# Optimization experiments

Hardware: AMD Instinct MI355X
Metric: run time of the kernel (lower is better)

Reference implementation:

```python
import jax, jax.numpy as jnp
import numpy as np

N, E = 20000, 320000
IN, HID, H, C, DFF, L = 256, 64, 4, 64, 128, 4  # per-head dim C = out_channels, concat width = H*C


def _init(k, shape, fan):
    return jax.random.normal(k, shape, jnp.float32) / np.float32(np.sqrt(fan))


def setup_inputs() -> dict:
    key = jax.random.key(0)
    ks = jax.random.split(key, 10)
    x = jax.random.normal(ks[0], (N, IN), jnp.float32)
    edge_index = jax.random.randint(ks[1], (2, E), 0, N)
    We = _init(ks[2], (IN, HID), IN)
    be = jnp.zeros((HID,), jnp.float32)
    Wc = _init(ks[3], (L, HID, H * C), HID)
    att_src = _init(ks[4], (L, H, C), C)
    att_dst = _init(ks[5], (L, H, C), C)
    bc = jnp.zeros((L, H * C), jnp.float32)
    W1 = _init(ks[6], (L, H * C, DFF), H * C)
    b1 = jnp.zeros((L, DFF), jnp.float32)
    W2 = _init(ks[7], (L, DFF, HID), DFF)
    b2 = jnp.zeros((L, HID), jnp.float32)
    ln_g = jnp.ones((L, HID), jnp.float32)
    ln_b = jnp.zeros((L, HID), jnp.float32)
    return dict(x=x, edge_index=edge_index, We=We, be=be, Wc=Wc, att_src=att_src,
                att_dst=att_dst, bc=bc, W1=W1, b1=b1, W2=W2, b2=b2, ln_g=ln_g, ln_b=ln_b)


def _layernorm(x, g, b, eps=1e-5):
    m = x.mean(-1, keepdims=True)
    v = ((x - m) ** 2).mean(-1, keepdims=True)
    return (x - m) / jnp.sqrt(v + eps) * g + b


def reference(x, edge_index, We, be, Wc, att_src, att_dst, bc, W1, b1, W2, b2, ln_g, ln_b):
    # dropout omitted (eval mode)
    n = x.shape[0]
    loops = jnp.arange(n, dtype=edge_index.dtype)
    src = jnp.concatenate([edge_index[0], loops])  # GATConv add_self_loops=True
    dst = jnp.concatenate([edge_index[1], loops])
    h = (x @ We + be) * jnp.sqrt(jnp.float32(HID))  # embed * sqrt(hidden)
    for l in range(L):  # small fixed layer loop
        xh = (h @ Wc[l]).reshape(n, H, C)          # [n,H,C]
        a_s = (xh * att_src[l]).sum(-1)            # [n,H]
        a_d = (xh * att_dst[l]).sum(-1)
        e = a_s[src] + a_d[dst]                    # [E+n,H]
        e = jnp.where(e > 0, e, 0.2 * e)           # leaky_relu(0.2)
        m = jax.ops.segment_max(e, dst, num_segments=n)
        e = jnp.exp(e - m[dst])
        z = jax.ops.segment_sum(e, dst, num_segments=n)
        alpha = e / (z[dst] + 1e-16)               # segment softmax over incoming edges
        msg = xh[src] * alpha[:, :, None]          # [E+n,H,C]
        out = jax.ops.segment_sum(msg, dst, num_segments=n).reshape(n, H * C) + bc[l]
        f = jax.nn.gelu(out @ W1[l] + b1[l], approximate=False) @ W2[l] + b2[l]
        h = h + _layernorm(f, ln_g[l], ln_b[l])    # residual
    return h  # last_hidden_state (head is None)
```

## Files before the change

### kernel.cpp

```cpp
#include <hip/hip_runtime.h>
#include <cmath>

#define NN   20000
#define NE   320000
#define IND  256
#define HIDD 64
#define NH   4
#define CD   64
#define HC   256
#define DFFD 128
#define NL   4


static __device__ __forceinline__ float lrelu(float v) { return v > 0.f ? v : 0.2f * v; }
static __device__ __forceinline__ float wsum(float v) { for (int k = 32; k; k >>= 1) v += __shfl_xor(v, k); return v; }
static __device__ __forceinline__ float wmax(float v) { for (int k = 32; k; k >>= 1) v = fmaxf(v, __shfl_xor(v, k)); return v; }

__global__ void ws_kernel(const float* __restrict__ Wc, const float* __restrict__ att_src,
                          const float* __restrict__ att_dst, float* __restrict__ ws_all) {
    int idx = blockIdx.x * 256 + threadIdx.x;
    int l = idx >> 9, r = (idx >> 6) & 7, k = idx & 63;
    int hh = r & 3;
    const float* att = ((r & 4) ? att_dst : att_src) + (size_t)l * NH * CD + hh * CD;
    const float* wrow = Wc + (size_t)l * HIDD * HC + (size_t)k * HC + hh * CD;
    float s = 0.f;
    for (int c = 0; c < CD; ++c) s += wrow[c] * att[c];
    ws_all[idx] = s;
}

__global__ __launch_bounds__(256) void embed_kernel(const float* __restrict__ x,
                                                    const float* __restrict__ We,
                                                    const float* __restrict__ be,
                                                    const float* __restrict__ ws_all,
                                                    float* __restrict__ h,
                                                    float* __restrict__ a_s, float* __restrict__ a_d) {
    __shared__ float s_x[16 * IND];
    const int base = blockIdx.x * 16, t = threadIdx.x;
    for (int idx = t; idx < 16 * IND / 4; idx += 256)
        ((float4*)s_x)[idx] = ((const float4*)(x + (size_t)base * IND))[idx];
    __syncthreads();
    const int c = t & 63, g = t >> 6;
    float acc[4] = {0.f, 0.f, 0.f, 0.f};
    const float4* sx4 = (const float4*)s_x;
#pragma unroll 2
    for (int k4 = 0; k4 < IND / 4; ++k4) {
        float w0 = We[(4 * k4 + 0) * HIDD + c];
        float w1 = We[(4 * k4 + 1) * HIDD + c];
        float w2 = We[(4 * k4 + 2) * HIDD + c];
        float w3 = We[(4 * k4 + 3) * HIDD + c];
#pragma unroll
        for (int i = 0; i < 4; ++i) {
            float4 v = sx4[(4 * g + i) * (IND / 4) + k4];
            acc[i] += v.x * w0 + v.y * w1 + v.z * w2 + v.w * w3;
        }
    }
    float bias = be[c];
    float wr[8];
#pragma unroll
    for (int r = 0; r < 8; ++r) wr[r] = ws_all[r * 64 + c];
#pragma unroll
    for (int i = 0; i < 4; ++i) {
        int node = base + 4 * g + i;
        float hv = (acc[i] + bias) * 8.0f;
        h[(size_t)node * HIDD + c] = hv;
        float s0 = wsum(hv * wr[0]), s1 = wsum(hv * wr[1]);
        float s2 = wsum(hv * wr[2]), s3 = wsum(hv * wr[3]);
        float s4 = wsum(hv * wr[4]), s5 = wsum(hv * wr[5]);
        float s6 = wsum(hv * wr[6]), s7 = wsum(hv * wr[7]);
        if (c == 0) {
            ((float4*)a_s)[node] = make_float4(s0, s1, s2, s3);
            ((float4*)a_d)[node] = make_float4(s4, s5, s6, s7);
        }
    }
}

__global__ void init_deg(int* __restrict__ deg, int* __restrict__ cursor) {
    int i = blockIdx.x * blockDim.x + threadIdx.x;
    if (i < NN) { deg[i] = 1; cursor[i] = 0; }
}

__global__ void count_edges(const int* __restrict__ ei, int* __restrict__ deg) {
    int e = blockIdx.x * blockDim.x + threadIdx.x;
    if (e < NE) atomicAdd(&deg[ei[NE + e]], 1);
}

__global__ void scan_kernel(const int* __restrict__ deg, int* __restrict__ rowptr) {
    __shared__ int part[1024];
    const int t = threadIdx.x;
    const int CH = (NN + 1023) / 1024;
    int lo = t * CH, hi = lo + CH; if (hi > NN) hi = NN;
    int s = 0;
    for (int i = lo; i < hi; ++i) s += deg[i];
    part[t] = s;
    __syncthreads();
    for (int off = 1; off < 1024; off <<= 1) {
        int v = 0;
        if (t >= off) v = part[t - off];
        __syncthreads();
        if (t >= off) part[t] += v;
        __syncthreads();
    }
    int base = (t == 0) ? 0 : part[t - 1];
    for (int i = lo; i < hi; ++i) { rowptr[i] = base; base += deg[i]; }
    if (lo <= NN - 1 && NN - 1 < hi) rowptr[NN] = base;
}

__global__ void scatter_edges(const int* __restrict__ ei, const int* __restrict__ rowptr,
                              int* __restrict__ cursor, int* __restrict__ csr_src) {
    int e = blockIdx.x * blockDim.x + threadIdx.x;
    if (e < NE) {
        int s = ei[e], d = ei[NE + e];
        int pos = atomicAdd(&cursor[d], 1);
        csr_src[rowptr[d] + pos] = s;
    } else if (e < NE + NN) {
        int i = e - NE;
        int pos = atomicAdd(&cursor[i], 1);
        csr_src[rowptr[i] + pos] = i;
    }
}

__global__ __launch_bounds__(256) void agg_kernel(
    const float* __restrict__ h, const float* __restrict__ a_s, const float* __restrict__ a_d,
    const int* __restrict__ rowptr, const int* __restrict__ csr_src,
    float* __restrict__ hagg) {
    __shared__ int    s_src[8][64];
    __shared__ float4 s_w[8][64];
    const int t = threadIdx.x, wave = t >> 6, lane = t & 63;
    const float4* as4 = (const float4*)a_s;
#pragma unroll
    for (int nd = 0; nd < 2; ++nd) {
        const int slot = wave * 2 + nd;
        const int i = blockIdx.x * 8 + slot;
        const int lo = rowptr[i], n = rowptr[i + 1] - lo;
        const float4 ad = ((const float4*)a_d)[i];
        float acc0 = 0.f, acc1 = 0.f, acc2 = 0.f, acc3 = 0.f;
        if (n <= 64) {
            float e0 = -1e30f, e1 = -1e30f, e2 = -1e30f, e3 = -1e30f;
            if (lane < n) {
                int s = csr_src[lo + lane];
                s_src[slot][lane] = s;
                float4 a = as4[s];
                e0 = lrelu(a.x + ad.x); e1 = lrelu(a.y + ad.y);
                e2 = lrelu(a.z + ad.z); e3 = lrelu(a.w + ad.w);
            }
            float M0 = wmax(e0), M1 = wmax(e1), M2 = wmax(e2), M3 = wmax(e3);
            float p0 = __expf(e0 - M0), p1 = __expf(e1 - M1);
            float p2 = __expf(e2 - M2), p3 = __expf(e3 - M3);
            float iz0 = 1.f / (wsum(p0) + 1e-16f), iz1 = 1.f / (wsum(p1) + 1e-16f);
            float iz2 = 1.f / (wsum(p2) + 1e-16f), iz3 = 1.f / (wsum(p3) + 1e-16f);
            if (lane < n) s_w[slot][lane] = make_float4(p0 * iz0, p1 * iz1, p2 * iz2, p3 * iz3);
            int j = 0;
            for (; j + 4 <= n; j += 4) {
                int  q0 = s_src[slot][j],     q1 = s_src[slot][j + 1];
                int  q2 = s_src[slot][j + 2], q3 = s_src[slot][j + 3];
                float h0 = h[(size_t)q0 * HIDD + lane], h1 = h[(size_t)q1 * HIDD + lane];
                float h2 = h[(size_t)q2 * HIDD + lane], h3 = h[(size_t)q3 * HIDD + lane];
                float4 w0 = s_w[slot][j],     w1 = s_w[slot][j + 1];
                float4 w2 = s_w[slot][j + 2], w3 = s_w[slot][j + 3];
                acc0 += h0 * w0.x + h1 * w1.x + h2 * w2.x + h3 * w3.x;
                acc1 += h0 * w0.y + h1 * w1.y + h2 * w2.y + h3 * w3.y;
                acc2 += h0 * w0.z + h1 * w1.z + h2 * w2.z + h3 * w3.z;
                acc3 += h0 * w0.w + h1 * w1.w + h2 * w2.w + h3 * w3.w;
            }
            for (; j < n; ++j) {
                float hv = h[(size_t)s_src[slot][j] * HIDD + lane];
                float4 w = s_w[slot][j];
                acc0 += hv * w.x; acc1 += hv * w.y; acc2 += hv * w.z; acc3 += hv * w.w;
            }
        } else {
            float m0 = -1e30f, m1 = -1e30f, m2 = -1e30f, m3 = -1e30f;
            for (int j = lane; j < n; j += 64) {
                int s = csr_src[lo + j];
                float4 a = as4[s];
                m0 = fmaxf(m0, lrelu(a.x + ad.x)); m1 = fmaxf(m1, lrelu(a.y + ad.y));
                m2 = fmaxf(m2, lrelu(a.z + ad.z)); m3 = fmaxf(m3, lrelu(a.w + ad.w));
            }
            m0 = wmax(m0); m1 = wmax(m1); m2 = wmax(m2); m3 = wmax(m3);
            float z0 = 0.f, z1 = 0.f, z2 = 0.f, z3 = 0.f;
            for (int j = lane; j < n; j += 64) {
                int s = csr_src[lo + j];
                float4 a = as4[s];
                z0 += __expf(lrelu(a.x + ad.x) - m0); z1 += __expf(lrelu(a.y + ad.y) - m1);
                z2 += __expf(lrelu(a.z + ad.z) - m2); z3 += __expf(lrelu(a.w + ad.w) - m3);
            }
            float iz0 = 1.f / (wsum(z0) + 1e-16f), iz1 = 1.f / (wsum(z1) + 1e-16f);
            float iz2 = 1.f / (wsum(z2) + 1e-16f), iz3 = 1.f / (wsum(z3) + 1e-16f);
            for (int cb = 0; cb < n; cb += 64) {
                int nn = n - cb; if (nn > 64) nn = 64;
                if (lane < nn) {
                    int s = csr_src[lo + cb + lane];
                    s_src[slot][lane] = s;
                    float4 a = as4[s];
                    s_w[slot][lane] = make_float4(__expf(lrelu(a.x + ad.x) - m0) * iz0,
                                                  __expf(lrelu(a.y + ad.y) - m1) * iz1,
                                                  __expf(lrelu(a.z + ad.z) - m2) * iz2,
                                                  __expf(lrelu(a.w + ad.w) - m3) * iz3);
                }
                int j = 0;
                for (; j + 4 <= nn; j += 4) {
                    int  q0 = s_src[slot][j],     q1 = s_src[slot][j + 1];
                    int  q2 = s_src[slot][j + 2], q3 = s_src[slot][j + 3];
                    float h0 = h[(size_t)q0 * HIDD + lane], h1 = h[(size_t)q1 * HIDD + lane];
                    float h2 = h[(size_t)q2 * HIDD + lane], h3 = h[(size_t)q3 * HIDD + lane];
                    float4 w0 = s_w[slot][j],     w1 = s_w[slot][j + 1];
                    float4 w2 = s_w[slot][j + 2], w3 = s_w[slot][j + 3];
                    acc0 += h0 * w0.x + h1 * w1.x + h2 * w2.x + h3 * w3.x;
                    acc1 += h0 * w0.y + h1 * w1.y + h2 * w2.y + h3 * w3.y;
                    acc2 += h0 * w0.z + h1 * w1.z + h2 * w2.z + h3 * w3.z;
                    acc3 += h0 * w0.w + h1 * w1.w + h2 * w2.w + h3 * w3.w;
                }
                for (; j < nn; ++j) {
                    float hv = h[(size_t)s_src[slot][j] * HIDD + lane];
                    float4 w = s_w[slot][j];
                    acc0 += hv * w.x; acc1 += hv * w.y; acc2 += hv * w.z; acc3 += hv * w.w;
                }
            }
        }
        float* hg = hagg + (size_t)i * HC;
        hg[0 * 64 + lane] = acc0; hg[1 * 64 + lane] = acc1;
        hg[2 * 64 + lane] = acc2; hg[3 * 64 + lane] = acc3;
    }
}

__global__ __launch_bounds__(256, 3) void ffn_kernel(
    const float* __restrict__ hagg, const float* __restrict__ Wc, const float* __restrict__ bc,
    const float* __restrict__ W1, const float* __restrict__ b1,
    const float* __restrict__ W2, const float* __restrict__ b2,
    const float* __restrict__ ln_g, const float* __restrict__ ln_b,
    const float* __restrict__ ws_next,
    float* __restrict__ h, float* __restrict__ a_s, float* __restrict__ a_d) {
    __shared__ float s_buf[8192];
    __shared__ float s_in[16 * HC];
    const int base = blockIdx.x * 16, t = threadIdx.x;
    for (int idx = t; idx < 16 * HC / 4; idx += 256)
        ((float4*)s_buf)[idx] = ((const float4*)(hagg + (size_t)base * HC))[idx];
    __syncthreads();

    {
        const int cq = t & 63, ng = t >> 6;
        const int c0 = cq * 4, hh = c0 >> 6;
        float4 acc[4];
#pragma unroll
        for (int i = 0; i < 4; ++i) acc[i] = make_float4(0.f, 0.f, 0.f, 0.f);
        const float* wbase = Wc + c0;
        const float4* sh4 = (const float4*)s_buf;
#pragma unroll 2
        for (int k4 = 0; k4 < 16; ++k4) {
            float4 w0 = *(const float4*)(wbase + (size_t)(4 * k4 + 0) * HC);
            float4 w1 = *(const float4*)(wbase + (size_t)(4 * k4 + 1) * HC);
            float4 w2 = *(const float4*)(wbase + (size_t)(4 * k4 + 2) * HC);
            float4 w3 = *(const float4*)(wbase + (size_t)(4 * k4 + 3) * HC);
#pragma unroll
            for (int i = 0; i < 4; ++i) {
                float4 v = sh4[(4 * ng + i) * 64 + hh * 16 + k4];
                acc[i].x += v.x * w0.x + v.y * w1.x + v.z * w2.x + v.w * w3.x;
                acc[i].y += v.x * w0.y + v.y * w1.y + v.z * w2.y + v.w * w3.y;
                acc[i].z += v.x * w0.z + v.y * w1.z + v.z * w2.z + v.w * w3.z;
                acc[i].w += v.x * w0.w + v.y * w1.w + v.z * w2.w + v.w * w3.w;
            }
        }
        float4 bb = *(const float4*)(bc + c0);
#pragma unroll
        for (int i = 0; i < 4; ++i) {
            float4 r = make_float4(acc[i].x + bb.x, acc[i].y + bb.y,
                                   acc[i].z + bb.z, acc[i].w + bb.w);
            *(float4*)(s_in + (size_t)(4 * ng + i) * HC + c0) = r;
        }
    }

    float acc1[8];
#pragma unroll
    for (int i = 0; i < 8; ++i) acc1[i] = 0.f;
    {
        const int f = t & 127, g = t >> 7;
        const float4* si4 = (const float4*)s_in;
        for (int kt = 0; kt < 4; ++kt) {
            __syncthreads();
            const float4* gsrc = (const float4*)(W1 + (size_t)kt * 64 * DFFD);
            for (int idx = t; idx < 2048; idx += 256)
                ((float4*)s_buf)[idx] = gsrc[idx];
            __syncthreads();
#pragma unroll 4
            for (int k4 = 0; k4 < 16; ++k4) {
                float w0 = s_buf[(4 * k4 + 0) * DFFD + f];
                float w1 = s_buf[(4 * k4 + 1) * DFFD + f];
                float w2 = s_buf[(4 * k4 + 2) * DFFD + f];
                float w3 = s_buf[(4 * k4 + 3) * DFFD + f];
#pragma unroll
                for (int i = 0; i < 8; ++i) {
                    float4 v = si4[(8 * g + i) * 64 + kt * 16 + k4];
                    acc1[i] += v.x * w0 + v.y * w1 + v.z * w2 + v.w * w3;
                }
            }
        }
        __syncthreads();
        float bb = b1[f];
#pragma unroll
        for (int i = 0; i < 8; ++i) {
            float d = acc1[i] + bb;
            s_buf[(8 * g + i) * DFFD + f] = 0.5f * d * (1.f + erff(d * 0.70710678118654752f));
        }
    }
    __syncthreads();

    {
        const int lane = t & 63, w = t >> 6;
        float acc[4];
#pragma unroll
        for (int i = 0; i < 4; ++i) acc[i] = 0.f;
        const float4* sm4 = (const float4*)s_buf;
#pragma unroll 4
        for (int k4 = 0; k4 < 32; ++k4) {
            float w0 = W2[(4 * k4 + 0) * HIDD + lane];
            float w1 = W2[(4 * k4 + 1) * HIDD + lane];
            float w2 = W2[(4 * k4 + 2) * HIDD + lane];
            float w3 = W2[(4 * k4 + 3) * HIDD + lane];
#pragma unroll
            for (int i = 0; i < 4; ++i) {
                float4 v = sm4[(4 * w + i) * 32 + k4];
                acc[i] += v.x * w0 + v.y * w1 + v.z * w2 + v.w * w3;
            }
        }
        const float b2c = b2[lane], gc = ln_g[lane], bbc = ln_b[lane];
        float wr[8];
#pragma unroll
        for (int r = 0; r < 8; ++r) wr[r] = 0.f;
        if (ws_next) {
#pragma unroll
            for (int r = 0; r < 8; ++r) wr[r] = ws_next[r * 64 + lane];
        }
#pragma unroll
        for (int i = 0; i < 4; ++i) {
            int node = base + 4 * w + i;
            float d = acc[i] + b2c;
            float mean = wsum(d) * (1.0f / 64.0f);
            float dd = d - mean;
            float var = wsum(dd * dd) * (1.0f / 64.0f);
            float hv = h[(size_t)node * HIDD + lane] + dd * rsqrtf(var + 1e-5f) * gc + bbc;
            h[(size_t)node * HIDD + lane] = hv;
            if (ws_next) {
                float s0 = wsum(hv * wr[0]), s1 = wsum(hv * wr[1]);
                float s2 = wsum(hv * wr[2]), s3 = wsum(hv * wr[3]);
                float s4 = wsum(hv * wr[4]), s5 = wsum(hv * wr[5]);
                float s6 = wsum(hv * wr[6]), s7 = wsum(hv * wr[7]);
                if (lane == 0) {
                    ((float4*)a_s)[node] = make_float4(s0, s1, s2, s3);
                    ((float4*)a_d)[node] = make_float4(s4, s5, s6, s7);
                }
            }
        }
    }
}

__global__ void copy_out(const float* __restrict__ h, float* __restrict__ out) {
    int i = blockIdx.x * blockDim.x + threadIdx.x;
    if (i < NN * HIDD / 4) ((float4*)out)[i] = ((const float4*)h)[i];
}

extern "C" void kernel_launch(void* const* d_in, const int* in_sizes, int n_in,
                              void* d_out, int out_size, void* d_ws, size_t ws_size,
                              hipStream_t stream) {
    const float* x       = (const float*)d_in[0];
    const int*   ei      = (const int*)d_in[1];
    const float* We      = (const float*)d_in[2];
    const float* be      = (const float*)d_in[3];
    const float* Wc      = (const float*)d_in[4];
    const float* att_src = (const float*)d_in[5];
    const float* att_dst = (const float*)d_in[6];
    const float* bc      = (const float*)d_in[7];
    const float* W1      = (const float*)d_in[8];
    const float* b1      = (const float*)d_in[9];
    const float* W2      = (const float*)d_in[10];
    const float* b2      = (const float*)d_in[11];
    const float* ln_g    = (const float*)d_in[12];
    const float* ln_b    = (const float*)d_in[13];

    char* ws = (char*)d_ws;
    size_t off = 0;
    auto alloc = [&](size_t bytes) -> void* {
        void* p = ws + off; off += (bytes + 255) & ~(size_t)255; return p;
    };
    float* h       = (float*)alloc((size_t)NN * HIDD * 4);
    float* hagg    = (float*)alloc((size_t)NN * HC * 4);
    float* a_s     = (float*)alloc((size_t)NN * NH * 4);
    float* a_d     = (float*)alloc((size_t)NN * NH * 4);
    float* ws_all  = (float*)alloc((size_t)NL * 8 * 64 * 4);
    int*   deg     = (int*)alloc((size_t)NN * 4);
    int*   rowptr  = (int*)alloc((size_t)(NN + 1) * 4);
    int*   cursor  = (int*)alloc((size_t)NN * 4);
    int*   csr_src = (int*)alloc((size_t)(NE + NN) * 4);
    (void)ws_size; (void)in_sizes; (void)n_in; (void)out_size;

    ws_kernel<<<8, 256, 0, stream>>>(Wc, att_src, att_dst, ws_all);
    init_deg<<<(NN + 255) / 256, 256, 0, stream>>>(deg, cursor);
    embed_kernel<<<NN / 16, 256, 0, stream>>>(x, We, be, ws_all, h, a_s, a_d);
    count_edges<<<(NE + 255) / 256, 256, 0, stream>>>(ei, deg);
    scan_kernel<<<1, 1024, 0, stream>>>(deg, rowptr);
    scatter_edges<<<(NE + NN + 255) / 256, 256, 0, stream>>>(ei, rowptr, cursor, csr_src);

    for (int l = 0; l < NL; ++l) {
        agg_kernel<<<NN / 8, 256, 0, stream>>>(h, a_s, a_d, rowptr, csr_src, hagg);
        ffn_kernel<<<NN / 16, 256, 0, stream>>>(hagg,
            Wc + (size_t)l * HIDD * HC, bc + (size_t)l * HC,
            W1 + (size_t)l * HC * DFFD, b1 + (size_t)l * DFFD,
            W2 + (size_t)l * DFFD * HIDD, b2 + (size_t)l * HIDD,
            ln_g + (size_t)l * HIDD, ln_b + (size_t)l * HIDD,
            (l + 1 < NL) ? (ws_all + (size_t)(l + 1) * 8 * 64) : (const float*)nullptr,
            h, a_s, a_d);
    }
    copy_out<<<(NN * HIDD / 4 + 255) / 256, 256, 0, stream>>>(h, (float*)d_out);
}
```

Measured before the change: 592.8 us.

## Process 32 nodes per FFN block with swizzled shared tiles and float4 W1 reads

The FFN kernel now handles 32 nodes per block instead of 16, so every weight load from Wc, W1 and W2 is reused across twice as many nodes. The aggregated input is stored in shared memory with a per-head rotation swizzle to spread LDS bank accesses. The W1 stage is remapped so each thread computes four output features as float4 for four nodes. This costs more registers and shared memory (launch bounds drop from 3 to 2 blocks per CU) and halves the number of blocks.

```diff
diff --git a/kernel.cpp b/kernel.cpp
--- a/kernel.cpp
+++ b/kernel.cpp
@@ -10,6 +10,7 @@
 #define HC   256
 #define DFFD 128
 #define NL   4
+#define NPB  32
 
 
 static __device__ __forceinline__ float lrelu(float v) { return v > 0.f ? v : 0.2f * v; }
@@ -222,103 +223,115 @@
     }
 }
 
-__global__ __launch_bounds__(256, 3) void ffn_kernel(
+__global__ __launch_bounds__(256, 2) void ffn_kernel(
     const float* __restrict__ hagg, const float* __restrict__ Wc, const float* __restrict__ bc,
     const float* __restrict__ W1, const float* __restrict__ b1,
     const float* __restrict__ W2, const float* __restrict__ b2,
     const float* __restrict__ ln_g, const float* __restrict__ ln_b,
     const float* __restrict__ ws_next,
     float* __restrict__ h, float* __restrict__ a_s, float* __restrict__ a_d) {
-    __shared__ float s_buf[8192];
-    __shared__ float s_in[16 * HC];
-    const int base = blockIdx.x * 16, t = threadIdx.x;
-    for (int idx = t; idx < 16 * HC / 4; idx += 256)
-        ((float4*)s_buf)[idx] = ((const float4*)(hagg + (size_t)base * HC))[idx];
+    __shared__ float s_A[8192];
+    __shared__ float s_B[8192];
+    float4* sA4 = (float4*)s_A;
+    float4* sB4 = (float4*)s_B;
+    const int base = blockIdx.x * NPB, t = threadIdx.x;
+
+    {
+        const float4* gsrc = (const float4*)(hagg + (size_t)base * HC);
+        for (int idx = t; idx < 2048; idx += 256) {
+            int n = idx >> 6, rem = idx & 63, hh = rem >> 4, k4 = rem & 15;
+            sA4[n * 64 + hh * 16 + ((k4 + 4 * hh) & 15)] = gsrc[idx];
+        }
+    }
     __syncthreads();
 
     {
-        const int cq = t & 63, ng = t >> 6;
-        const int c0 = cq * 4, hh = c0 >> 6;
-        float4 acc[4];
-#pragma unroll
-        for (int i = 0; i < 4; ++i) acc[i] = make_float4(0.f, 0.f, 0.f, 0.f);
-        const float* wbase = Wc + c0;
-        const float4* sh4 = (const float4*)s_buf;
+        const int cg = t & 63, ng = t >> 6, hh = cg >> 4;
+        float4 acc[8];
+#pragma unroll
+        for (int i = 0; i < 8; ++i) acc[i] = make_float4(0.f, 0.f, 0.f, 0.f);
+        const float* wbase = Wc + 4 * cg;
 #pragma unroll 2
         for (int k4 = 0; k4 < 16; ++k4) {
             float4 w0 = *(const float4*)(wbase + (size_t)(4 * k4 + 0) * HC);
             float4 w1 = *(const float4*)(wbase + (size_t)(4 * k4 + 1) * HC);
             float4 w2 = *(const float4*)(wbase + (size_t)(4 * k4 + 2) * HC);
             float4 w3 = *(const float4*)(wbase + (size_t)(4 * k4 + 3) * HC);
-#pragma unroll
-            for (int i = 0; i < 4; ++i) {
-                float4 v = sh4[(4 * ng + i) * 64 + hh * 16 + k4];
+            const int koff = hh * 16 + ((k4 + 4 * hh) & 15);
+#pragma unroll
+            for (int i = 0; i < 8; ++i) {
+                float4 v = sA4[(8 * ng + i) * 64 + koff];
                 acc[i].x += v.x * w0.x + v.y * w1.x + v.z * w2.x + v.w * w3.x;
                 acc[i].y += v.x * w0.y + v.y * w1.y + v.z * w2.y + v.w * w3.y;
                 acc[i].z += v.x * w0.z + v.y * w1.z + v.z * w2.z + v.w * w3.z;
                 acc[i].w += v.x * w0.w + v.y * w1.w + v.z * w2.w + v.w * w3.w;
             }
         }
-        float4 bb = *(const float4*)(bc + c0);
+        float4 bb = *(const float4*)(bc + 4 * cg);
+#pragma unroll
+        for (int i = 0; i < 8; ++i)
+            sB4[(8 * ng + i) * 64 + cg] = make_float4(acc[i].x + bb.x, acc[i].y + bb.y,
+                                                      acc[i].z + bb.z, acc[i].w + bb.w);
+    }
+    __syncthreads();
+
+    const int fg = t & 31, ng2 = t >> 5;
+    float4 acc1[4];
+#pragma unroll
+    for (int i = 0; i < 4; ++i) acc1[i] = make_float4(0.f, 0.f, 0.f, 0.f);
+    for (int kt = 0; kt < 4; ++kt) {
+        {
+            const float4* gsrc = (const float4*)(W1 + (size_t)kt * 64 * DFFD);
+            for (int idx = t; idx < 2048; idx += 256) sA4[idx] = gsrc[idx];
+        }
+        __syncthreads();
+#pragma unroll 4
+        for (int k4 = 0; k4 < 16; ++k4) {
+            float4 wt0 = sA4[(4 * k4 + 0) * 32 + fg];
+            float4 wt1 = sA4[(4 * k4 + 1) * 32 + fg];
+            float4 wt2 = sA4[(4 * k4 + 2) * 32 + fg];
+            float4 wt3 = sA4[(4 * k4 + 3) * 32 + fg];
+#pragma unroll
+            for (int i = 0; i < 4; ++i) {
+                float4 v = sB4[(4 * ng2 + i) * 64 + kt * 16 + k4];
+                acc1[i].x += v.x * wt0.x + v.y * wt1.x + v.z * wt2.x + v.w * wt3.x;
+                acc1[i].y += v.x * wt0.y + v.y * wt1.y + v.z * wt2.y + v.w * wt3.y;
+                acc1[i].z += v.x * wt0.z + v.y * wt1.z + v.z * wt2.z + v.w * wt3.z;
+                acc1[i].w += v.x * wt0.w + v.y * wt1.w + v.z * wt2.w + v.w * wt3.w;
+            }
+        }
+        __syncthreads();
+    }
+    {
+        float4 bb = *(const float4*)(b1 + 4 * fg);
 #pragma unroll
         for (int i = 0; i < 4; ++i) {
-            float4 r = make_float4(acc[i].x + bb.x, acc[i].y + bb.y,
-                                   acc[i].z + bb.z, acc[i].w + bb.w);
-            *(float4*)(s_in + (size_t)(4 * ng + i) * HC + c0) = r;
-        }
-    }
-
-    float acc1[8];
-#pragma unroll
-    for (int i = 0; i < 8; ++i) acc1[i] = 0.f;
-    {
-        const int f = t & 127, g = t >> 7;
-        const float4* si4 = (const float4*)s_in;
-        for (int kt = 0; kt < 4; ++kt) {
-            __syncthreads();
-            const float4* gsrc = (const float4*)(W1 + (size_t)kt * 64 * DFFD);
-            for (int idx = t; idx < 2048; idx += 256)
-                ((float4*)s_buf)[idx] = gsrc[idx];
-            __syncthreads();
-#pragma unroll 4
-            for (int k4 = 0; k4 < 16; ++k4) {
-                float w0 = s_buf[(4 * k4 + 0) * DFFD + f];
-                float w1 = s_buf[(4 * k4 + 1) * DFFD + f];
-                float w2 = s_buf[(4 * k4 + 2) * DFFD + f];
-                float w3 = s_buf[(4 * k4 + 3) * DFFD + f];
-#pragma unroll
-                for (int i = 0; i < 8; ++i) {
-                    float4 v = si4[(8 * g + i) * 64 + kt * 16 + k4];
-                    acc1[i] += v.x * w0 + v.y * w1 + v.z * w2 + v.w * w3;
-                }
-            }
-        }
-        __syncthreads();
-        float bb = b1[f];
-#pragma unroll
-        for (int i = 0; i < 8; ++i) {
-            float d = acc1[i] + bb;
-            s_buf[(8 * g + i) * DFFD + f] = 0.5f * d * (1.f + erff(d * 0.70710678118654752f));
+            float dx = acc1[i].x + bb.x, dy = acc1[i].y + bb.y;
+            float dz = acc1[i].z + bb.z, dw = acc1[i].w + bb.w;
+            sA4[(4 * ng2 + i) * 32 + fg] = make_float4(
+                0.5f * dx * (1.f + erff(dx * 0.70710678118654752f)),
+                0.5f * dy * (1.f + erff(dy * 0.70710678118654752f)),
+                0.5f * dz * (1.f + erff(dz * 0.70710678118654752f)),
+                0.5f * dw * (1.f + erff(dw * 0.70710678118654752f)));
         }
     }
     __syncthreads();
 
     {
         const int lane = t & 63, w = t >> 6;
-        float acc[4];
-#pragma unroll
-        for (int i = 0; i < 4; ++i) acc[i] = 0.f;
-        const float4* sm4 = (const float4*)s_buf;
-#pragma unroll 4
+        float acc2[8];
+#pragma unroll
+        for (int i = 0; i < 8; ++i) acc2[i] = 0.f;
+#pragma unroll 2
         for (int k4 = 0; k4 < 32; ++k4) {
             float w0 = W2[(4 * k4 + 0) * HIDD + lane];
             float w1 = W2[(4 * k4 + 1) * HIDD + lane];
             float w2 = W2[(4 * k4 + 2) * HIDD + lane];
             float w3 = W2[(4 * k4 + 3) * HIDD + lane];
 #pragma unroll
-            for (int i = 0; i < 4; ++i) {
-                float4 v = sm4[(4 * w + i) * 32 + k4];
-                acc[i] += v.x * w0 + v.y * w1 + v.z * w2 + v.w * w3;
+            for (int i = 0; i < 8; ++i) {
+                float4 v = sA4[(8 * w + i) * 32 + k4];
+                acc2[i] += v.x * w0 + v.y * w1 + v.z * w2 + v.w * w3;
             }
         }
         const float b2c = b2[lane], gc = ln_g[lane], bbc = ln_b[lane];
@@ -330,9 +343,9 @@
             for (int r = 0; r < 8; ++r) wr[r] = ws_next[r * 64 + lane];
         }
 #pragma unroll
-        for (int i = 0; i < 4; ++i) {
-            int node = base + 4 * w + i;
-            float d = acc[i] + b2c;
+        for (int i = 0; i < 8; ++i) {
+            int node = base + 8 * w + i;
+            float d = acc2[i] + b2c;
             float mean = wsum(d) * (1.0f / 64.0f);
             float dd = d - mean;
             float var = wsum(dd * dd) * (1.0f / 64.0f);
@@ -400,7 +413,7 @@
 
     for (int l = 0; l < NL; ++l) {
         agg_kernel<<<NN / 8, 256, 0, stream>>>(h, a_s, a_d, rowptr, csr_src, hagg);
-        ffn_kernel<<<NN / 16, 256, 0, stream>>>(hagg,
+        ffn_kernel<<<NN / NPB, 256, 0, stream>>>(hagg,
             Wc + (size_t)l * HIDD * HC, bc + (size_t)l * HC,
             W1 + (size_t)l * HC * DFFD, b1 + (size_t)l * DFFD,
             W2 + (size_t)l * DFFD * HIDD, b2 + (size_t)l * HIDD,
```

Measured after the change: 570.8 us. -3.7%, faster.

## Fold per-head Wc projection into W1 via precomputed block-diagonal product

Applied to the files above, without the earlier changes.

The aggregation already works on h (hidden dim) per head, so the FFN kernel first applied Wc per head and then W1. This change precomputes W1eff[l] = blockdiag(Wc head slices) @ W1 and b1eff = bc @ W1 + b1 in small setup kernels, and the FFN feeds hagg straight into the W1eff matmul. That removes one dense projection stage and a shared-memory round trip per layer. The cost is two extra tiny launches and a different floating-point summation order.

```diff
diff --git a/kernel.cpp b/kernel.cpp
--- a/kernel.cpp
+++ b/kernel.cpp
@@ -26,6 +26,29 @@
     float s = 0.f;
     for (int c = 0; c < CD; ++c) s += wrow[c] * att[c];
     ws_all[idx] = s;
+}
+
+__global__ void w1eff_kernel(const float* __restrict__ Wc, const float* __restrict__ W1,
+                             float* __restrict__ W1eff) {
+    const int b = blockIdx.x;
+    const int l = b >> 8, hk = b & 255, hh = hk >> 6, kl = hk & 63;
+    const int f = threadIdx.x;
+    const float* wc = Wc + (size_t)l * HIDD * HC + (size_t)kl * HC + hh * 64;
+    const float* w1 = W1 + (size_t)l * HC * DFFD + (size_t)(hh * 64) * DFFD + f;
+    float s = 0.f;
+#pragma unroll 4
+    for (int c = 0; c < 64; ++c) s += wc[c] * w1[(size_t)c * DFFD];
+    W1eff[(size_t)l * HC * DFFD + (size_t)hk * DFFD + f] = s;
+}
+
+__global__ void b1eff_kernel(const float* __restrict__ bc, const float* __restrict__ W1,
+                             const float* __restrict__ b1, float* __restrict__ b1eff) {
+    const int l = blockIdx.x, f = threadIdx.x;
+    const float* w1 = W1 + (size_t)l * HC * DFFD + f;
+    const float* bcl = bc + (size_t)l * HC;
+    float s = b1[(size_t)l * DFFD + f];
+    for (int c = 0; c < HC; ++c) s += bcl[c] * w1[(size_t)c * DFFD];
+    b1eff[l * DFFD + f] = s;
 }
 
 __global__ __launch_bounds__(256) void embed_kernel(const float* __restrict__ x,
@@ -223,8 +246,7 @@
 }
 
 __global__ __launch_bounds__(256, 3) void ffn_kernel(
-    const float* __restrict__ hagg, const float* __restrict__ Wc, const float* __restrict__ bc,
-    const float* __restrict__ W1, const float* __restrict__ b1,
+    const float* __restrict__ hagg, const float* __restrict__ W1eff, const float* __restrict__ b1eff,
     const float* __restrict__ W2, const float* __restrict__ b2,
     const float* __restrict__ ln_g, const float* __restrict__ ln_b,
     const float* __restrict__ ws_next,
@@ -233,50 +255,17 @@
     __shared__ float s_in[16 * HC];
     const int base = blockIdx.x * 16, t = threadIdx.x;
     for (int idx = t; idx < 16 * HC / 4; idx += 256)
-        ((float4*)s_buf)[idx] = ((const float4*)(hagg + (size_t)base * HC))[idx];
-    __syncthreads();
-
-    {
-        const int cq = t & 63, ng = t >> 6;
-        const int c0 = cq * 4, hh = c0 >> 6;
-        float4 acc[4];
-#pragma unroll
-        for (int i = 0; i < 4; ++i) acc[i] = make_float4(0.f, 0.f, 0.f, 0.f);
-        const float* wbase = Wc + c0;
-        const float4* sh4 = (const float4*)s_buf;
-#pragma unroll 2
-        for (int k4 = 0; k4 < 16; ++k4) {
-            float4 w0 = *(const float4*)(wbase + (size_t)(4 * k4 + 0) * HC);
-            float4 w1 = *(const float4*)(wbase + (size_t)(4 * k4 + 1) * HC);
-            float4 w2 = *(const float4*)(wbase + (size_t)(4 * k4 + 2) * HC);
-            float4 w3 = *(const float4*)(wbase + (size_t)(4 * k4 + 3) * HC);
-#pragma unroll
-            for (int i = 0; i < 4; ++i) {
-                float4 v = sh4[(4 * ng + i) * 64 + hh * 16 + k4];
-                acc[i].x += v.x * w0.x + v.y * w1.x + v.z * w2.x + v.w * w3.x;
-                acc[i].y += v.x * w0.y + v.y * w1.y + v.z * w2.y + v.w * w3.y;
-                acc[i].z += v.x * w0.z + v.y * w1.z + v.z * w2.z + v.w * w3.z;
-                acc[i].w += v.x * w0.w + v.y * w1.w + v.z * w2.w + v.w * w3.w;
-            }
-        }
-        float4 bb = *(const float4*)(bc + c0);
-#pragma unroll
-        for (int i = 0; i < 4; ++i) {
-            float4 r = make_float4(acc[i].x + bb.x, acc[i].y + bb.y,
-                                   acc[i].z + bb.z, acc[i].w + bb.w);
-            *(float4*)(s_in + (size_t)(4 * ng + i) * HC + c0) = r;
-        }
-    }
-
+        ((float4*)s_in)[idx] = ((const float4*)(hagg + (size_t)base * HC))[idx];
+
+    const int f = t & 127, g = t >> 7;
     float acc1[8];
 #pragma unroll
     for (int i = 0; i < 8; ++i) acc1[i] = 0.f;
     {
-        const int f = t & 127, g = t >> 7;
         const float4* si4 = (const float4*)s_in;
         for (int kt = 0; kt < 4; ++kt) {
             __syncthreads();
-            const float4* gsrc = (const float4*)(W1 + (size_t)kt * 64 * DFFD);
+            const float4* gsrc = (const float4*)(W1eff + (size_t)kt * 64 * DFFD);
             for (int idx = t; idx < 2048; idx += 256)
                 ((float4*)s_buf)[idx] = gsrc[idx];
             __syncthreads();
@@ -294,7 +283,7 @@
             }
         }
         __syncthreads();
-        float bb = b1[f];
+        float bb = b1eff[f];
 #pragma unroll
         for (int i = 0; i < 8; ++i) {
             float d = acc1[i] + bb;
@@ -385,6 +374,8 @@
     float* a_s     = (float*)alloc((size_t)NN * NH * 4);
     float* a_d     = (float*)alloc((size_t)NN * NH * 4);
     float* ws_all  = (float*)alloc((size_t)NL * 8 * 64 * 4);
+    float* W1eff   = (float*)alloc((size_t)NL * HC * DFFD * 4);
+    float* b1eff   = (float*)alloc((size_t)NL * DFFD * 4);
     int*   deg     = (int*)alloc((size_t)NN * 4);
     int*   rowptr  = (int*)alloc((size_t)(NN + 1) * 4);
     int*   cursor  = (int*)alloc((size_t)NN * 4);
@@ -392,6 +383,8 @@
     (void)ws_size; (void)in_sizes; (void)n_in; (void)out_size;
 
     ws_kernel<<<8, 256, 0, stream>>>(Wc, att_src, att_dst, ws_all);
+    w1eff_kernel<<<NL * 256, 128, 0, stream>>>(Wc, W1, W1eff);
+    b1eff_kernel<<<NL, 128, 0, stream>>>(bc, W1, b1, b1eff);
     init_deg<<<(NN + 255) / 256, 256, 0, stream>>>(deg, cursor);
     embed_kernel<<<NN / 16, 256, 0, stream>>>(x, We, be, ws_all, h, a_s, a_d);
     count_edges<<<(NE + 255) / 256, 256, 0, stream>>>(ei, deg);
@@ -401,8 +394,7 @@
     for (int l = 0; l < NL; ++l) {
         agg_kernel<<<NN / 8, 256, 0, stream>>>(h, a_s, a_d, rowptr, csr_src, hagg);
         ffn_kernel<<<NN / 16, 256, 0, stream>>>(hagg,
-            Wc + (size_t)l * HIDD * HC, bc + (size_t)l * HC,
-            W1 + (size_t)l * HC * DFFD, b1 + (size_t)l * DFFD,
+            W1eff + (size_t)l * HC * DFFD, b1eff + (size_t)l * DFFD,
             W2 + (size_t)l * DFFD * HIDD, b2 + (size_t)l * HIDD,
             ln_g + (size_t)l * HIDD, ln_b + (size_t)l * HIDD,
             (l + 1 < NL) ? (ws_all + (size_t)(l + 1) * 8 * 64) : (const float*)nullptr,
```

After: 565.6 us. 4.6% less time.
